# Kernel optimization log

Hardware: AMD Instinct MI355X
Metric: run time of the kernel (lower is better)

## Reference

```python
import jax, jax.numpy as jnp
import numpy as np

N_NODES = 100000
N_EDGES = 1600000
D = 128


def setup_inputs() -> dict:
    key = jax.random.key(0)
    ks = jax.random.split(key, 9)
    inp = {
        "embs": jax.random.normal(ks[0], (N_NODES, D), dtype=jnp.float32),
        "edge_index0": jax.random.randint(ks[1], (2, N_EDGES), 0, N_NODES, dtype=jnp.int64 if jax.config.jax_enable_x64 else jnp.int32),
        "edge_index1": jax.random.randint(ks[2], (2, N_EDGES), 0, N_NODES, dtype=jnp.int64 if jax.config.jax_enable_x64 else jnp.int32),
        "w_l0": jax.random.normal(ks[3], (D, D), dtype=jnp.float32) * (1.0 / np.sqrt(D)),
        "w_r0": jax.random.normal(ks[4], (D, D), dtype=jnp.float32) * (1.0 / np.sqrt(D)),
        "b0": jnp.zeros((D,), dtype=jnp.float32),
        "w_l1": jax.random.normal(ks[5], (D, D), dtype=jnp.float32) * (1.0 / np.sqrt(D)),
        "w_r1": jax.random.normal(ks[6], (D, D), dtype=jnp.float32) * (1.0 / np.sqrt(D)),
        "b1": jnp.zeros((D,), dtype=jnp.float32),
    }
    return inp


def _sage_conv(x, edge_index, w_l, w_r, b):
    # PyG SAGEConv: out[i] = lin_l(mean_{j->i} x[j]) + lin_r(x[i])
    src, dst = edge_index[0], edge_index[1]
    n = x.shape[0]
    msg = jnp.take(x, src, axis=0)                                  # [E, D] gather
    summed = jax.ops.segment_sum(msg, dst, num_segments=n)          # [N, D] scatter-add
    cnt = jax.ops.segment_sum(jnp.ones(src.shape, x.dtype), dst, num_segments=n)
    agg = summed / jnp.maximum(cnt, 1.0)[:, None]                   # mean; 0 for isolated nodes
    return agg @ w_l.T + b + x @ w_r.T


def reference(embs, edge_index0, edge_index1, w_l0, w_r0, b0, w_l1, w_r1, b1):
    # layer 0 (not last): dropout (eval -> identity) + GELU (torch default = exact erf)
    x = _sage_conv(embs, edge_index0, w_l0, w_r0, b0)
    x = jax.nn.gelu(x, approximate=False)
    # layer 1 (last): no dropout / activation
    x = _sage_conv(x, edge_index1, w_l1, w_r1, b1)
    return x
```

## Files before the change

kernel.cpp:

```cpp
#include <hip/hip_runtime.h>
#include <hip/hip_fp16.h>
#include <math.h>

#define D 128
#define SH 9
#define BW (1 << SH)
#define EPT 16

typedef _Float16 half4v __attribute__((ext_vector_type(4)));
typedef _Float16 half8  __attribute__((ext_vector_type(8)));
typedef float    floatx16 __attribute__((ext_vector_type(16)));

typedef __attribute__((address_space(3))) uint32_t lds_u32_t;
typedef const __attribute__((address_space(1))) uint32_t g_u32_t;

__global__ __launch_bounds__(256) void cast_half(
        const float* __restrict__ x, _Float16* __restrict__ y, int n) {
    int i = blockIdx.x * 256 + threadIdx.x;
    int idx = i * 4;
    if (idx >= n) return;
    float4 v = *(const float4*)(x + idx);
    half4v h;
    h[0] = (_Float16)v.x; h[1] = (_Float16)v.y;
    h[2] = (_Float16)v.z; h[3] = (_Float16)v.w;
    *(half4v*)(y + idx) = h;
}

__global__ __launch_bounds__(256) void prep_bswz(
        const float* __restrict__ wl, const float* __restrict__ wr,
        _Float16* __restrict__ B) {
    int idx = blockIdx.x * 256 + threadIdx.x;
    if (idx >= 64 * 512) return;
    int j = idx & 7;
    int lane = (idx >> 3) & 63;
    int f = idx >> 9;
    int ks = f >> 2, cb = f & 3;
    int k = ks * 16 + (lane >> 5) * 8 + j;
    int c = cb * 32 + (lane & 31);
    float v = (k < 128) ? wl[c * 128 + k] : wr[c * 128 + (k - 128)];
    B[idx] = (_Float16)v;
}

__global__ __launch_bounds__(256) void hist_coarse(
        const int* __restrict__ ei0, const int* __restrict__ ei1,
        int E, int NBK, int* __restrict__ ccnt) {
    __shared__ int h[512];
    int NBIN = 2 * NBK;
    int t = threadIdx.x;
    h[t] = 0; h[t + 256] = 0;
    __syncthreads();
    int t0 = blockIdx.x * (256 * EPT) + t;
#pragma unroll
    for (int k = 0; k < EPT; ++k) {
        int idx = t0 + k * 256;
        if (idx < 2 * E) {
            int g = idx >= E;
            int e = idx - g * E;
            int dst = (g ? ei1 : ei0)[E + e];
            atomicAdd(&h[g * NBK + (dst >> SH)], 1);
        }
    }
    __syncthreads();
    for (int b = t; b < NBIN; b += 256)
        if (h[b]) atomicAdd(&ccnt[b * 16], h[b]);
}

__global__ __launch_bounds__(256) void scan_coarse(
        const int* __restrict__ ccnt, int NBK, int E, int N,
        int* __restrict__ gbase, int* __restrict__ gcur,
        int* __restrict__ rp0, int* __restrict__ rp1) {
    __shared__ int part[256];
    int t = threadIdx.x;
    for (int g = 0; g < 2; ++g) {
        int v = (t < NBK) ? ccnt[(g * NBK + t) * 16] : 0;
        part[t] = v;
        __syncthreads();
        for (int off = 1; off < 256; off <<= 1) {
            int u = (t >= off) ? part[t - off] : 0;
            __syncthreads();
            part[t] += u;
            __syncthreads();
        }
        if (t < NBK) {
            int ex = (t == 0) ? 0 : part[t - 1];
            int b = g * NBK + t;
            gbase[b] = ex;
            gcur[b * 16] = ex;
        }
        __syncthreads();
    }
    if (t == 0) { rp0[N] = E; rp1[N] = E; }
}

__global__ __launch_bounds__(256) void bin_pass1(
        const int* __restrict__ ei0, const int* __restrict__ ei1,
        int E, int NBK, int* __restrict__ gcur,
        int* __restrict__ stage0, int* __restrict__ stage1) {
    __shared__ int cnt[512];
    __shared__ int base[512];
    int NBIN = 2 * NBK;
    int t = threadIdx.x;
    cnt[t] = 0; cnt[t + 256] = 0;
    __syncthreads();
    int t0 = blockIdx.x * (256 * EPT) + t;
    int pk[EPT];
    int bn[EPT];
#pragma unroll
    for (int k = 0; k < EPT; ++k) {
        int idx = t0 + k * 256;
        bn[k] = -1;
        if (idx < 2 * E) {
            int g = idx >= E;
            int e = idx - g * E;
            const int* ei = g ? ei1 : ei0;
            int src = ei[e];
            int dst = ei[E + e];
            pk[k] = src | ((dst & (BW - 1)) << 17);
            bn[k] = g * NBK + (dst >> SH);
            atomicAdd(&cnt[bn[k]], 1);
        }
    }
    __syncthreads();
    for (int b = t; b < NBIN; b += 256) {
        int c = cnt[b];
        base[b] = c ? atomicAdd(&gcur[b * 16], c) : 0;
        cnt[b] = 0;
    }
    __syncthreads();
#pragma unroll
    for (int k = 0; k < EPT; ++k) {
        if (bn[k] >= 0) {
            int b = bn[k];
            int r = atomicAdd(&cnt[b], 1);
            int* stage = (b >= NBK) ? stage1 : stage0;
            stage[base[b] + r] = pk[k];
        }
    }
}

__global__ __launch_bounds__(256) void bin_pass2(
        const int* __restrict__ gbase,
        const int* __restrict__ stage0, const int* __restrict__ stage1,
        int* __restrict__ rp0, int* __restrict__ rp1,
        int* __restrict__ es0, int* __restrict__ es1,
        int N, int NBK, int E) {
    __shared__ int cnt[BW];
    __shared__ int part[256];
    int b = blockIdx.x;
    int g = b >= NBK;
    int bk = b - g * NBK;
    const int* stage = g ? stage1 : stage0;
    int* rp = g ? rp1 : rp0;
    int* es = g ? es1 : es0;
    int lo = bk << SH;
    int hi = min(lo + BW, N);
    int nd = hi - lo;
    int beg = gbase[b];
    int end = (bk == NBK - 1) ? E : gbase[b + 1];
    int t = threadIdx.x;
    cnt[t] = 0; cnt[t + 256] = 0;
    __syncthreads();
    for (int i = beg + t; i < end; i += 256)
        atomicAdd(&cnt[(unsigned)stage[i] >> 17], 1);
    __syncthreads();
    int c0 = cnt[t * 2], c1 = cnt[t * 2 + 1];
    part[t] = c0 + c1;
    __syncthreads();
    for (int off = 1; off < 256; off <<= 1) {
        int u = (t >= off) ? part[t - off] : 0;
        __syncthreads();
        part[t] += u;
        __syncthreads();
    }
    int ex = (t == 0) ? 0 : part[t - 1];
    int base0 = beg + ex;
    if (t * 2 < nd)     rp[lo + t * 2]     = base0;
    if (t * 2 + 1 < nd) rp[lo + t * 2 + 1] = base0 + c0;
    __syncthreads();
    cnt[t * 2] = base0;
    cnt[t * 2 + 1] = base0 + c0;
    __syncthreads();
    int i = beg + t;
    for (; i + 768 < end; i += 1024) {
        unsigned p0 = (unsigned)stage[i];
        unsigned p1 = (unsigned)stage[i + 256];
        unsigned p2 = (unsigned)stage[i + 512];
        unsigned p3 = (unsigned)stage[i + 768];
        int q0 = atomicAdd(&cnt[p0 >> 17], 1);
        int q1 = atomicAdd(&cnt[p1 >> 17], 1);
        int q2 = atomicAdd(&cnt[p2 >> 17], 1);
        int q3 = atomicAdd(&cnt[p3 >> 17], 1);
        es[q0] = p0 & 0x1FFFF;
        es[q1] = p1 & 0x1FFFF;
        es[q2] = p2 & 0x1FFFF;
        es[q3] = p3 & 0x1FFFF;
    }
    for (; i < end; i += 256) {
        unsigned p = (unsigned)stage[i];
        int q = atomicAdd(&cnt[p >> 17], 1);
        es[q] = p & 0x1FFFF;
    }
}

__global__ __launch_bounds__(256) void agg_half(
        const _Float16* __restrict__ x, const int* __restrict__ row_ptr,
        const int* __restrict__ edge_src, _Float16* __restrict__ agg, int N) {
    int gt = blockIdx.x * 256 + threadIdx.x;
    int w = gt >> 6;
    int lane = gt & 63;
    if (w >= N) return;
    int beg = row_ptr[w];
    int end = row_ptr[w + 1];
    int grp = lane >> 5;
    int c   = lane & 31;
    unsigned co = (unsigned)c * 8u;
    const char* xb = (const char*)x;
    float ax = 0.f, ay = 0.f, az = 0.f, aw = 0.f;
    float one = 1.0f;

    for (int chunk = beg; chunk < end; chunk += 64) {
        int n = min(64, end - chunk);
        int iv = (lane < n) ? edge_src[chunk + lane] : -1;
        for (int e = 0; e < n; e += 8) {
            int s[4];
            uint2 v[4];
#pragma unroll
            for (int j = 0; j < 4; ++j)
                s[j] = __shfl(iv, e + 2 * j + grp);
#pragma unroll
            for (int j = 0; j < 4; ++j) {
                v[j] = make_uint2(0u, 0u);
                if (s[j] >= 0)
                    v[j] = *(const uint2*)(xb + (unsigned)s[j] * 256u + co);
            }
#pragma unroll
            for (int j = 0; j < 4; ++j) {
                asm("v_fma_mix_f32 %0, %1, %2, %0 op_sel:[0,0,0] op_sel_hi:[1,0,0]"
                    : "+v"(ax) : "v"(v[j].x), "v"(one));
                asm("v_fma_mix_f32 %0, %1, %2, %0 op_sel:[1,0,0] op_sel_hi:[1,0,0]"
                    : "+v"(ay) : "v"(v[j].x), "v"(one));
                asm("v_fma_mix_f32 %0, %1, %2, %0 op_sel:[0,0,0] op_sel_hi:[1,0,0]"
                    : "+v"(az) : "v"(v[j].y), "v"(one));
                asm("v_fma_mix_f32 %0, %1, %2, %0 op_sel:[1,0,0] op_sel_hi:[1,0,0]"
                    : "+v"(aw) : "v"(v[j].y), "v"(one));
            }
        }
    }

    ax += __shfl_xor(ax, 32);
    ay += __shfl_xor(ay, 32);
    az += __shfl_xor(az, 32);
    aw += __shfl_xor(aw, 32);

    int deg = end - beg;
    float inv = (deg > 0) ? 1.0f / (float)deg : 0.0f;
    if (lane < 32) {
        half4v h;
        h[0] = (_Float16)(ax * inv);
        h[1] = (_Float16)(ay * inv);
        h[2] = (_Float16)(az * inv);
        h[3] = (_Float16)(aw * inv);
        *(half4v*)((char*)agg + (size_t)w * 256 + co) = h;
    }
}

__device__ __forceinline__ float gelu_fast(float v) {
    float z = v * 0.70710678118654752f;
    float s = fabsf(z);
    float t = __builtin_amdgcn_rcpf(fmaf(0.3275911f, s, 1.0f));
    float poly = t * fmaf(t, fmaf(t, fmaf(t, fmaf(t, 1.061405429f,
                      -1.453152027f), 1.421413741f), -0.284496736f),
                      0.254829592f);
    float e = __builtin_amdgcn_exp2f(-1.4426950408889634f * s * s);
    float erfv = copysignf(fmaf(-poly, e, 1.0f), z);
    return 0.5f * v * (1.0f + erfv);
}

template <bool GELU, typename OutT>
__global__ __launch_bounds__(256, 2) void sage_mfma(
        const _Float16* __restrict__ aggh, const _Float16* __restrict__ xh,
        const _Float16* __restrict__ Bswz, const float* __restrict__ bias,
        OutT* __restrict__ out, int N) {
    __shared__ uint4 a_lds[64 * 65];

    const int tid = threadIdx.x;
    const int n0 = blockIdx.x * 128;
    const int wave = tid >> 6;
    const int lane = tid & 63;
    const int l31 = lane & 31;
    const int lhi = lane >> 5;
    const int wr = wave >> 1;
    const int wc = wave & 1;

    if (n0 + 128 <= N) {
#pragma unroll
        for (int i = 0; i < 16; ++i) {
            int c = wave * 16 + i;
            const _Float16* srcb = (c < 32) ? aggh : xh;
            int r0 = n0 + 4 * (c & 31);
            const char* g = (const char*)srcb + (size_t)r0 * 256 + lane * 16;
            uint32_t* l = (uint32_t*)((char*)a_lds + c * 1040);
            __builtin_amdgcn_global_load_lds((g_u32_t*)g, (lds_u32_t*)l,
                                             16, 0, 0);
        }
    } else {
#pragma unroll
        for (int i = 0; i < 16; ++i) {
            int c = wave * 16 + i;
            const _Float16* srcb = (c < 32) ? aggh : xh;
            int grow = n0 + 4 * (c & 31) + (lane >> 4);
            uint4 v = make_uint4(0u, 0u, 0u, 0u);
            if (grow < N)
                v = *(const uint4*)((const char*)srcb + (size_t)grow * 256
                                    + (lane & 15) * 16);
            *(uint4*)((char*)a_lds + c * 1040 + lane * 16) = v;
        }
    }

    half8 breg[2][8][2];
#pragma unroll
    for (int ph = 0; ph < 2; ++ph)
#pragma unroll
        for (int ks = 0; ks < 8; ++ks)
#pragma unroll
            for (int c2 = 0; c2 < 2; ++c2)
                breg[ph][ks][c2] = *(const half8*)(
                    Bswz + (size_t)ph * 16384
                         + ((ks * 4) + (wc * 2 + c2)) * 512 + lane * 8);
#pragma unroll
    for (int ph = 0; ph < 2; ++ph)
#pragma unroll
        for (int ks = 0; ks < 8; ++ks)
#pragma unroll
            for (int c2 = 0; c2 < 2; ++c2)
                asm volatile("" : "+v"(breg[ph][ks][c2]));

    floatx16 acc[2][2];
#pragma unroll
    for (int r2 = 0; r2 < 2; ++r2)
#pragma unroll
        for (int c2 = 0; c2 < 2; ++c2)
#pragma unroll
            for (int r = 0; r < 16; ++r) acc[r2][c2][r] = 0.0f;

    __syncthreads();

#pragma unroll
    for (int ph = 0; ph < 2; ++ph)
#pragma unroll
        for (int ks = 0; ks < 8; ++ks)
#pragma unroll
            for (int r2 = 0; r2 < 2; ++r2) {
                int r = ph * 128 + (wr * 2 + r2) * 32 + l31;
                int abyte = (r >> 2) * 1040 + (r & 3) * 256
                            + ks * 32 + lhi * 16;
                half8 af = *(const half8*)((const char*)a_lds + abyte);
                acc[r2][0] = __builtin_amdgcn_mfma_f32_32x32x16_f16(
                    af, breg[ph][ks][0], acc[r2][0], 0, 0, 0);
                acc[r2][1] = __builtin_amdgcn_mfma_f32_32x32x16_f16(
                    af, breg[ph][ks][1], acc[r2][1], 0, 0, 0);
            }

#pragma unroll
    for (int r2 = 0; r2 < 2; ++r2)
#pragma unroll
        for (int c2 = 0; c2 < 2; ++c2) {
            int col = (wc * 2 + c2) * 32 + l31;
            float bv = bias[col];
#pragma unroll
            for (int r = 0; r < 16; ++r) {
                int rowin = (r & 3) + 8 * (r >> 2) + 4 * lhi;
                int grow = n0 + (wr * 2 + r2) * 32 + rowin;
                if (grow < N) {
                    float v = acc[r2][c2][r] + bv;
                    if (GELU) v = gelu_fast(v);
                    out[(size_t)grow * 128 + col] = (OutT)v;
                }
            }
        }
}

extern "C" void kernel_launch(void* const* d_in, const int* in_sizes, int n_in,
                              void* d_out, int out_size, void* d_ws, size_t ws_size,
                              hipStream_t stream) {
    const float* embs = (const float*)d_in[0];
    const int*   ei0  = (const int*)d_in[1];
    const int*   ei1  = (const int*)d_in[2];
    const float* w_l0 = (const float*)d_in[3];
    const float* w_r0 = (const float*)d_in[4];
    const float* b0   = (const float*)d_in[5];
    const float* w_l1 = (const float*)d_in[6];
    const float* w_r1 = (const float*)d_in[7];
    const float* b1   = (const float*)d_in[8];
    float* out = (float*)d_out;

    const int N = in_sizes[0] / D;
    const int E = in_sizes[1] / 2;
    const int NBK = (N + BW - 1) >> SH;
    const int NBIN = 2 * NBK;

    _Float16* x_h   = (_Float16*)d_ws;
    _Float16* h_h   = x_h + (size_t)N * D;
    _Float16* agg_h = h_h + (size_t)N * D;
    _Float16* Bswz0 = agg_h + (size_t)N * D;
    _Float16* Bswz1 = Bswz0 + 64 * 512;
    int* rp0   = (int*)(Bswz1 + 64 * 512);
    int* rp1   = rp0 + (N + 1);
    int* es0   = rp1 + (N + 1);
    int* es1   = es0 + E;
    int* ccnt  = es1 + E;
    int* gbase = ccnt + NBIN * 16;
    int* gcur  = gbase + NBIN;
    int* stage0 = (int*)agg_h;
    int* stage1 = stage0 + E;

    const int cast_grid = ((size_t)N * D / 4 + 255) / 256;
    const int bin_grid  = (2 * E + 256 * EPT - 1) / (256 * EPT);
    const int agg_grid  = ((size_t)N * 64 + 255) / 256;
    const int gemm_grid = (N + 127) / 128;

    cast_half<<<cast_grid, 256, 0, stream>>>(embs, x_h, N * D);
    prep_bswz<<<128, 256, 0, stream>>>(w_l0, w_r0, Bswz0);
    prep_bswz<<<128, 256, 0, stream>>>(w_l1, w_r1, Bswz1);

    hipMemsetAsync(ccnt, 0, (size_t)NBIN * 16 * sizeof(int), stream);
    hist_coarse<<<bin_grid, 256, 0, stream>>>(ei0, ei1, E, NBK, ccnt);
    scan_coarse<<<1, 256, 0, stream>>>(ccnt, NBK, E, N, gbase, gcur, rp0, rp1);
    bin_pass1<<<bin_grid, 256, 0, stream>>>(ei0, ei1, E, NBK, gcur,
                                            stage0, stage1);
    bin_pass2<<<NBIN, 256, 0, stream>>>(gbase, stage0, stage1,
                                        rp0, rp1, es0, es1, N, NBK, E);

    agg_half<<<agg_grid, 256, 0, stream>>>(x_h, rp0, es0, agg_h, N);
    sage_mfma<true, _Float16><<<gemm_grid, 256, 0, stream>>>(
        agg_h, x_h, Bswz0, b0, h_h, N);

    agg_half<<<agg_grid, 256, 0, stream>>>(h_h, rp1, es1, agg_h, N);
    sage_mfma<false, float><<<gemm_grid, 256, 0, stream>>>(
        agg_h, h_h, Bswz1, b1, out, N);
}
```

Baseline: 399.1 us.

## Halve GEMM row tile to 64 and merge weight-swizzle launches

The MFMA SAGE GEMM kernel now processes 64 rows per block instead of 128. Each wave handles one 32-row tile instead of two, which halves LDS use and the accumulator registers and raises the launch-bounds occupancy hint from 2 to 3 blocks. The grid doubles, so each block reloads the preloaded B fragments for half as much work. Separately, the two prep_bswz launches are fused into a single launch that handles both layers, saving one kernel launch.

```diff
diff --git a/kernel.cpp b/kernel.cpp
--- a/kernel.cpp
+++ b/kernel.cpp
@@ -26,11 +26,17 @@
     *(half4v*)(y + idx) = h;
 }
 
-__global__ __launch_bounds__(256) void prep_bswz(
-        const float* __restrict__ wl, const float* __restrict__ wr,
-        _Float16* __restrict__ B) {
-    int idx = blockIdx.x * 256 + threadIdx.x;
-    if (idx >= 64 * 512) return;
+__global__ __launch_bounds__(256) void prep_bswz2(
+        const float* __restrict__ wl0, const float* __restrict__ wr0,
+        const float* __restrict__ wl1, const float* __restrict__ wr1,
+        _Float16* __restrict__ B0, _Float16* __restrict__ B1) {
+    int gid = blockIdx.x * 256 + threadIdx.x;
+    if (gid >= 2 * 64 * 512) return;
+    int layer = gid >> 15;
+    int idx = gid & 32767;
+    const float* wl = layer ? wl1 : wl0;
+    const float* wr = layer ? wr1 : wr0;
+    _Float16* B = layer ? B1 : B0;
     int j = idx & 7;
     int lane = (idx >> 3) & 63;
     int f = idx >> 9;
@@ -277,14 +283,14 @@
 }
 
 template <bool GELU, typename OutT>
-__global__ __launch_bounds__(256, 2) void sage_mfma(
+__global__ __launch_bounds__(256, 3) void sage_mfma(
         const _Float16* __restrict__ aggh, const _Float16* __restrict__ xh,
         const _Float16* __restrict__ Bswz, const float* __restrict__ bias,
         OutT* __restrict__ out, int N) {
-    __shared__ uint4 a_lds[64 * 65];
+    __shared__ uint4 a_lds[32 * 65];
 
     const int tid = threadIdx.x;
-    const int n0 = blockIdx.x * 128;
+    const int n0 = blockIdx.x * 64;
     const int wave = tid >> 6;
     const int lane = tid & 63;
     const int l31 = lane & 31;
@@ -292,12 +298,12 @@
     const int wr = wave >> 1;
     const int wc = wave & 1;
 
-    if (n0 + 128 <= N) {
-#pragma unroll
-        for (int i = 0; i < 16; ++i) {
-            int c = wave * 16 + i;
-            const _Float16* srcb = (c < 32) ? aggh : xh;
-            int r0 = n0 + 4 * (c & 31);
+    if (n0 + 64 <= N) {
+#pragma unroll
+        for (int i = 0; i < 8; ++i) {
+            int c = wave * 8 + i;
+            const _Float16* srcb = (c < 16) ? aggh : xh;
+            int r0 = n0 + 4 * (c & 15);
             const char* g = (const char*)srcb + (size_t)r0 * 256 + lane * 16;
             uint32_t* l = (uint32_t*)((char*)a_lds + c * 1040);
             __builtin_amdgcn_global_load_lds((g_u32_t*)g, (lds_u32_t*)l,
@@ -305,10 +311,10 @@
         }
     } else {
 #pragma unroll
-        for (int i = 0; i < 16; ++i) {
-            int c = wave * 16 + i;
-            const _Float16* srcb = (c < 32) ? aggh : xh;
-            int grow = n0 + 4 * (c & 31) + (lane >> 4);
+        for (int i = 0; i < 8; ++i) {
+            int c = wave * 8 + i;
+            const _Float16* srcb = (c < 16) ? aggh : xh;
+            int grow = n0 + 4 * (c & 15) + (lane >> 4);
             uint4 v = make_uint4(0u, 0u, 0u, 0u);
             if (grow < N)
                 v = *(const uint4*)((const char*)srcb + (size_t)grow * 256
@@ -335,49 +341,43 @@
             for (int c2 = 0; c2 < 2; ++c2)
                 asm volatile("" : "+v"(breg[ph][ks][c2]));
 
-    floatx16 acc[2][2];
-#pragma unroll
-    for (int r2 = 0; r2 < 2; ++r2)
-#pragma unroll
-        for (int c2 = 0; c2 < 2; ++c2)
-#pragma unroll
-            for (int r = 0; r < 16; ++r) acc[r2][c2][r] = 0.0f;
+    floatx16 acc[2];
+#pragma unroll
+    for (int c2 = 0; c2 < 2; ++c2)
+#pragma unroll
+        for (int r = 0; r < 16; ++r) acc[c2][r] = 0.0f;
 
     __syncthreads();
 
 #pragma unroll
     for (int ph = 0; ph < 2; ++ph)
 #pragma unroll
-        for (int ks = 0; ks < 8; ++ks)
-#pragma unroll
-            for (int r2 = 0; r2 < 2; ++r2) {
-                int r = ph * 128 + (wr * 2 + r2) * 32 + l31;
-                int abyte = (r >> 2) * 1040 + (r & 3) * 256
-                            + ks * 32 + lhi * 16;
-                half8 af = *(const half8*)((const char*)a_lds + abyte);
-                acc[r2][0] = __builtin_amdgcn_mfma_f32_32x32x16_f16(
-                    af, breg[ph][ks][0], acc[r2][0], 0, 0, 0);
-                acc[r2][1] = __builtin_amdgcn_mfma_f32_32x32x16_f16(
-                    af, breg[ph][ks][1], acc[r2][1], 0, 0, 0);
+        for (int ks = 0; ks < 8; ++ks) {
+            int r = ph * 64 + wr * 32 + l31;
+            int abyte = (r >> 2) * 1040 + (r & 3) * 256
+                        + ks * 32 + lhi * 16;
+            half8 af = *(const half8*)((const char*)a_lds + abyte);
+            acc[0] = __builtin_amdgcn_mfma_f32_32x32x16_f16(
+                af, breg[ph][ks][0], acc[0], 0, 0, 0);
+            acc[1] = __builtin_amdgcn_mfma_f32_32x32x16_f16(
+                af, breg[ph][ks][1], acc[1], 0, 0, 0);
+        }
+
+#pragma unroll
+    for (int c2 = 0; c2 < 2; ++c2) {
+        int col = (wc * 2 + c2) * 32 + l31;
+        float bv = bias[col];
+#pragma unroll
+        for (int r = 0; r < 16; ++r) {
+            int rowin = (r & 3) + 8 * (r >> 2) + 4 * lhi;
+            int grow = n0 + wr * 32 + rowin;
+            if (grow < N) {
+                float v = acc[c2][r] + bv;
+                if (GELU) v = gelu_fast(v);
+                out[(size_t)grow * 128 + col] = (OutT)v;
             }
-
-#pragma unroll
-    for (int r2 = 0; r2 < 2; ++r2)
-#pragma unroll
-        for (int c2 = 0; c2 < 2; ++c2) {
-            int col = (wc * 2 + c2) * 32 + l31;
-            float bv = bias[col];
-#pragma unroll
-            for (int r = 0; r < 16; ++r) {
-                int rowin = (r & 3) + 8 * (r >> 2) + 4 * lhi;
-                int grow = n0 + (wr * 2 + r2) * 32 + rowin;
-                if (grow < N) {
-                    float v = acc[r2][c2][r] + bv;
-                    if (GELU) v = gelu_fast(v);
-                    out[(size_t)grow * 128 + col] = (OutT)v;
-                }
-            }
-        }
+        }
+    }
 }
 
 extern "C" void kernel_launch(void* const* d_in, const int* in_sizes, int n_in,
@@ -417,11 +417,10 @@
     const int cast_grid = ((size_t)N * D / 4 + 255) / 256;
     const int bin_grid  = (2 * E + 256 * EPT - 1) / (256 * EPT);
     const int agg_grid  = ((size_t)N * 64 + 255) / 256;
-    const int gemm_grid = (N + 127) / 128;
+    const int gemm_grid = (N + 63) / 64;
 
     cast_half<<<cast_grid, 256, 0, stream>>>(embs, x_h, N * D);
-    prep_bswz<<<128, 256, 0, stream>>>(w_l0, w_r0, Bswz0);
-    prep_bswz<<<128, 256, 0, stream>>>(w_l1, w_r1, Bswz1);
+    prep_bswz2<<<256, 256, 0, stream>>>(w_l0, w_r0, w_l1, w_r1, Bswz0, Bswz1);
 
     hipMemsetAsync(ccnt, 0, (size_t)NBIN * 16 * sizeof(int), stream);
     hist_coarse<<<bin_grid, 256, 0, stream>>>(ei0, ei1, E, NBK, ccnt);
```

Result: faster. 388.7 us (-2.6%).
